# Performance work log

Hardware: AMD Instinct MI355X
Metric: run time of the kernel (lower is better)

The kernel has to match this reference:

```python
import jax, jax.numpy as jnp
import numpy as np

DIM = 512
NUM_LATENTS = 128
TRUE_BATCH = 8
DOWNSCALING = 16


def setup_inputs() -> dict:
    key = jax.random.key(0)
    ks = jax.random.split(key, 7)
    B = TRUE_BATCH * NUM_LATENTS
    s = 0.02
    return {
        "x": jax.random.normal(ks[0], (B, DOWNSCALING, DIM), dtype=jnp.float32),
        "l": jax.random.normal(ks[1], (B, NUM_LATENTS, DIM), dtype=jnp.float32),
        "Wq": jax.random.normal(ks[2], (DIM, DIM), dtype=jnp.float32) * s,
        "Wk": jax.random.normal(ks[3], (DIM, DIM), dtype=jnp.float32) * s,
        "Wv": jax.random.normal(ks[4], (DIM, DIM), dtype=jnp.float32) * s,
        "Wo": jax.random.normal(ks[5], (DIM, DIM), dtype=jnp.float32) * s,
        "bo": jax.random.normal(ks[6], (DIM,), dtype=jnp.float32) * s,
        "num_heads": 8,
    }


def reference(x, l, Wq, Wk, Wv, Wo, bo, num_heads):
    B, n_tok, d = x.shape
    num_latents = l.shape[1]
    dh = d // num_heads

    def split_heads(t):
        # (b, n, h*d) -> (b, h, n, d)
        b, n, _ = t.shape
        return t.reshape(b, n, num_heads, dh).transpose(0, 2, 1, 3)

    q = split_heads(x @ Wq.T)   # (B, h, n_tok, dh)
    k = split_heads(l @ Wk.T)   # (B, h, num_latents, dh)
    v = split_heads(l @ Wv.T)

    scores = jnp.einsum('bhid,bhjd->bhij', q, k) * (dh ** -0.5)

    # mask row for batch element b is row (b mod num_latents) of a causal triu mask:
    # latent index m may attend only to latents j <= m.
    row = jnp.arange(B) % num_latents                       # (B,)
    allowed = jnp.arange(num_latents)[None, :] <= row[:, None]  # (B, num_latents)
    mask = jnp.where(allowed, 0.0, -jnp.inf).astype(scores.dtype)

    scores = scores + mask[:, None, None, :]
    attn = jax.nn.softmax(scores, axis=-1)

    out = jnp.einsum('bhij,bhjd->bhid', attn, v)            # (B, h, n_tok, dh)
    out = out.transpose(0, 2, 1, 3).reshape(B, n_tok, d)
    return out @ Wo.T + bo
```

## Files before the change

kernel.cpp:

```cpp
#include <hip/hip_runtime.h>


typedef __bf16 bf16;
typedef __attribute__((ext_vector_type(8))) __bf16 bf16x8;
typedef __attribute__((ext_vector_type(4))) __bf16 bf16x4;
typedef __attribute__((ext_vector_type(4))) float  float4v;

#define MFMA16(a, b, c) __builtin_amdgcn_mfma_f32_16x16x32_bf16((a), (b), (c), 0, 0, 0)

__device__ __forceinline__ void gl2lds16(const bf16* g, bf16* l) {
    __builtin_amdgcn_global_load_lds(
        (const __attribute__((address_space(1))) void*)g,
        (__attribute__((address_space(3))) void*)l, 16, 0, 0);
}

__global__ __launch_bounds__(256) void cast_f32_bf16(const float* __restrict__ src,
                                                     bf16* __restrict__ dst, int n4) {
    const int stride = gridDim.x * 256;
    for (int i = blockIdx.x * 256 + threadIdx.x; i < n4; i += stride) {
        float4v f = ((const float4v*)src)[i];
        ((bf16x4*)dst)[i] = bf16x4{(bf16)f.x, (bf16)f.y, (bf16)f.z, (bf16)f.w};
    }
}

__global__ __launch_bounds__(256) void cast_weights(const float* __restrict__ Wq,
                                                    const float* __restrict__ Wk,
                                                    const float* __restrict__ Wv,
                                                    const float* __restrict__ Wo,
                                                    bf16* __restrict__ Wq_b,
                                                    bf16* __restrict__ Wkv_b,
                                                    bf16* __restrict__ Wo_b) {
    const int i = blockIdx.x * 256 + threadIdx.x;
    const int w = i >> 16;
    const int j = i & 65535;
    const float* src = (w == 0) ? Wq : (w == 1) ? Wk : (w == 2) ? Wv : Wo;
    bf16x4* dst = (w == 0) ? (bf16x4*)Wq_b
                : (w == 1) ? (bf16x4*)Wkv_b
                : (w == 2) ? ((bf16x4*)Wkv_b) + 65536
                           : (bf16x4*)Wo_b;
    float4v f = ((const float4v*)src)[j];
    dst[j] = bf16x4{(bf16)f.x, (bf16)f.y, (bf16)f.z, (bf16)f.w};
}

template <int MODE>
__global__ __launch_bounds__(256) void gemm_bt(const bf16* __restrict__ A,
                                               const bf16* __restrict__ W,
                                               void* __restrict__ C0,
                                               void* __restrict__ C1,
                                               const float* __restrict__ bias,
                                               int nT, int mPerXcd) {
    __shared__ alignas(16) bf16 Asl[128 * 32];
    __shared__ alignas(16) bf16 Bsl[128 * 32];

    const int bid = blockIdx.x;
    const int xcd = bid & 7;
    const int s   = bid >> 3;
    const int mt  = xcd * mPerXcd + s / nT;
    const int nt  = s % nT;
    const int m0  = mt * 128;
    const int n0  = nt * 128;

    const int tid  = threadIdx.x;
    const int wave = tid >> 6;
    const int lane = tid & 63;
    const int mi   = lane & 15;
    const int quad = lane >> 4;
    const int qrow = (wave >> 1) * 64;
    const int qcol = (wave & 1) * 64;

    const int srow = wave * 16 + (lane >> 2);
    const int scol = (lane & 3) * 8;

    float4v acc[4][4] = {};

    for (int kt = 0; kt < 16; ++kt) {
        const int k0 = kt * 32;
#pragma unroll
        for (int r = 0; r < 2; ++r) {
            gl2lds16(A + (size_t)(m0 + srow + r * 64) * 512 + k0 + scol,
                     &Asl[wave * 512 + r * 2048]);
            gl2lds16(W + (size_t)(n0 + srow + r * 64) * 512 + k0 + scol,
                     &Bsl[wave * 512 + r * 2048]);
        }
        __syncthreads();

        bf16x8 af[4], bfr[4];
#pragma unroll
        for (int i = 0; i < 4; ++i)
            af[i] = *(const bf16x8*)&Asl[(qrow + i * 16 + mi) * 32 + quad * 8];
#pragma unroll
        for (int j = 0; j < 4; ++j)
            bfr[j] = *(const bf16x8*)&Bsl[(qcol + j * 16 + mi) * 32 + quad * 8];
#pragma unroll
        for (int i = 0; i < 4; ++i)
#pragma unroll
            for (int j = 0; j < 4; ++j)
                acc[i][j] = MFMA16(af[i], bfr[j], acc[i][j]);
        __syncthreads();
    }

    if (MODE == 1 && nt >= 4) {
        const size_t b = (size_t)mt;
#pragma unroll
        for (int i = 0; i < 4; ++i) {
            const int lat0 = qrow + i * 16 + quad * 4;
#pragma unroll
            for (int j = 0; j < 4; ++j) {
                const int dd = (n0 - 512) + qcol + j * 16 + mi;
                bf16x4 o = {(bf16)acc[i][j][0], (bf16)acc[i][j][1],
                            (bf16)acc[i][j][2], (bf16)acc[i][j][3]};
                *(bf16x4*)((bf16*)C1 + (b * 512 + dd) * 128 + lat0) = o;
            }
        }
        return;
    }
#pragma unroll
    for (int i = 0; i < 4; ++i) {
#pragma unroll
        for (int j = 0; j < 4; ++j) {
            const int row = m0 + qrow + i * 16 + quad * 4;
            const int col = n0 + qcol + j * 16 + mi;
#pragma unroll
            for (int r = 0; r < 4; ++r) {
                float v = acc[i][j][r];
                if (MODE == 2)
                    ((float*)C0)[(size_t)(row + r) * 512 + col] = v + bias[col];
                else
                    ((bf16*)C0)[(size_t)(row + r) * 512 + col] = (bf16)v;
            }
        }
    }
}

__global__ __launch_bounds__(256) void attn_kernel(const bf16* __restrict__ Q,
                                                   const bf16* __restrict__ K,
                                                   const bf16* __restrict__ Vt,
                                                   bf16* __restrict__ O) {
    __shared__ alignas(16) bf16 Plds[4][16 * 136];

    const int w      = threadIdx.x >> 6;
    const int bh     = blockIdx.x * 4 + w;
    const int b      = bh >> 3;
    const int h      = bh & 7;
    const int rowb   = b & 127;
    const int ntiles = (rowb >> 4) + 1;
    const int nkt    = (ntiles + 1) >> 1;
    const int lane   = threadIdx.x & 63;
    const int mi     = lane & 15;
    const int quad   = lane >> 4;

    const bf16* qbase = Q + (size_t)(b * 16 + mi) * 512 + h * 64 + quad * 8;
    const bf16x8 aq0 = *(const bf16x8*)(qbase);
    const bf16x8 aq1 = *(const bf16x8*)(qbase + 32);

    float4v sc[8];
    const bf16* kbase = K + (size_t)(b * 128 + mi) * 512 + h * 64 + quad * 8;
#pragma unroll
    for (int jt = 0; jt < 8; ++jt) {
        if (jt < ntiles) {
            const bf16* kb = kbase + (size_t)jt * 16 * 512;
            bf16x8 bk0 = *(const bf16x8*)(kb);
            bf16x8 bk1 = *(const bf16x8*)(kb + 32);
            float4v a = {};
            a = MFMA16(aq0, bk0, a);
            a = MFMA16(aq1, bk1, a);
            sc[jt] = a;
        }
    }

#pragma unroll
    for (int jt = 0; jt < 8; ++jt) {
        if (jt < ntiles) {
            const bool masked = (jt * 16 + mi) > rowb;
#pragma unroll
            for (int r = 0; r < 4; ++r)
                sc[jt][r] = masked ? -1e30f : sc[jt][r] * 0.125f;
        }
    }

#pragma unroll
    for (int r = 0; r < 4; ++r) {
        float mx = sc[0][r];
#pragma unroll
        for (int jt = 1; jt < 8; ++jt)
            if (jt < ntiles) mx = fmaxf(mx, sc[jt][r]);
#pragma unroll
        for (int off = 1; off < 16; off <<= 1) mx = fmaxf(mx, __shfl_xor(mx, off, 64));
        float s = 0.f;
#pragma unroll
        for (int jt = 0; jt < 8; ++jt) {
            if (jt < ntiles) {
                float p = __expf(sc[jt][r] - mx);
                sc[jt][r] = p;
                s += p;
            }
        }
#pragma unroll
        for (int off = 1; off < 16; off <<= 1) s += __shfl_xor(s, off, 64);
        const float inv = 1.f / s;
#pragma unroll
        for (int jt = 0; jt < 8; ++jt) {
            if (jt < 2 * nkt) {
                float p = (jt < ntiles) ? sc[jt][r] * inv : 0.f;
                Plds[w][(quad * 4 + r) * 136 + jt * 16 + mi] = (bf16)p;
            }
        }
    }
    __syncthreads();

    float4v ao[4] = {};
    const bf16* vb0 = Vt + ((size_t)b * 512 + h * 64) * 128;
#pragma unroll
    for (int ks = 0; ks < 4; ++ks) {
        if (ks < nkt) {
            bf16x8 ap = *(const bf16x8*)&Plds[w][mi * 136 + ks * 32 + quad * 8];
#pragma unroll
            for (int jt = 0; jt < 4; ++jt) {
                bf16x8 bv = *(const bf16x8*)(vb0 + (size_t)(jt * 16 + mi) * 128
                                             + ks * 32 + quad * 8);
                ao[jt] = MFMA16(ap, bv, ao[jt]);
            }
        }
    }

#pragma unroll
    for (int jt = 0; jt < 4; ++jt)
#pragma unroll
        for (int r = 0; r < 4; ++r)
            O[(size_t)(b * 16 + quad * 4 + r) * 512 + h * 64 + jt * 16 + mi] =
                (bf16)ao[jt][r];
}

extern "C" void kernel_launch(void* const* d_in, const int* in_sizes, int n_in,
                              void* d_out, int out_size, void* d_ws, size_t ws_size,
                              hipStream_t stream) {
    const float* x  = (const float*)d_in[0];
    const float* l  = (const float*)d_in[1];
    const float* Wq = (const float*)d_in[2];
    const float* Wk = (const float*)d_in[3];
    const float* Wv = (const float*)d_in[4];
    const float* Wo = (const float*)d_in[5];
    const float* bo = (const float*)d_in[6];

    char* ws = (char*)d_ws;
    size_t off = 0;
    bf16* Wq_b  = (bf16*)(ws + off); off += (size_t)512 * 512 * 2;
    bf16* Wo_b  = (bf16*)(ws + off); off += (size_t)512 * 512 * 2;
    bf16* Wkv_b = (bf16*)(ws + off); off += (size_t)1024 * 512 * 2;
    bf16* xb    = (bf16*)(ws + off); off += (size_t)16384 * 512 * 2;
    bf16* lb    = (bf16*)(ws + off); off += (size_t)131072 * 512 * 2;
    bf16* Qb    = (bf16*)(ws + off); off += (size_t)16384 * 512 * 2;
    bf16* Kb    = (bf16*)(ws + off); off += (size_t)131072 * 512 * 2;
    bf16* Vtb   = (bf16*)(ws + off); off += (size_t)1024 * 512 * 128 * 2;
    bf16* AOb   = (bf16*)(ws + off);

    cast_weights<<<1024, 256, 0, stream>>>(Wq, Wk, Wv, Wo, Wq_b, Wkv_b, Wo_b);
    cast_f32_bf16<<<2048, 256, 0, stream>>>(x, xb, 16384 * 512 / 4);
    cast_f32_bf16<<<8192, 256, 0, stream>>>(l, lb, 131072 * 512 / 4);

    gemm_bt<0><<<512,  256, 0, stream>>>(xb, Wq_b,  Qb, nullptr, nullptr, 4, 16);
    gemm_bt<1><<<8192, 256, 0, stream>>>(lb, Wkv_b, Kb, Vtb,     nullptr, 8, 128);

    attn_kernel<<<2048, 256, 0, stream>>>(Qb, Kb, Vtb, AOb);

    gemm_bt<2><<<512, 256, 0, stream>>>(AOb, Wo_b, d_out, nullptr, bo, 4, 16);
}
```

Measured before the change: 713.3 us.

## Add dedicated 256x256 K/V projection GEMM with 4-stage LDS pipeline

Replaces the generic 128x128 K/V GEMM with a specialized kernel that computes 256x256 output tiles using 8 waves per block. It adds a 4-slot LDS ring filled by direct global-to-LDS loads, XOR swizzling to avoid bank conflicts, explicit waitcnt and barrier scheduling, and raised priority around the MFMA sections. The goal is more operand reuse per LDS byte and loads that overlap with compute in the largest GEMM. The cost is heavy LDS use of about 128 KB per block, which limits occupancy, plus fragile hand-written synchronization.

```diff
diff --git a/kernel.cpp b/kernel.cpp
--- a/kernel.cpp
+++ b/kernel.cpp
@@ -46,7 +46,6 @@
 __global__ __launch_bounds__(256) void gemm_bt(const bf16* __restrict__ A,
                                                const bf16* __restrict__ W,
                                                void* __restrict__ C0,
-                                               void* __restrict__ C1,
                                                const float* __restrict__ bias,
                                                int nT, int mPerXcd) {
     __shared__ alignas(16) bf16 Asl[128 * 32];
@@ -99,21 +98,6 @@
         __syncthreads();
     }
 
-    if (MODE == 1 && nt >= 4) {
-        const size_t b = (size_t)mt;
-#pragma unroll
-        for (int i = 0; i < 4; ++i) {
-            const int lat0 = qrow + i * 16 + quad * 4;
-#pragma unroll
-            for (int j = 0; j < 4; ++j) {
-                const int dd = (n0 - 512) + qcol + j * 16 + mi;
-                bf16x4 o = {(bf16)acc[i][j][0], (bf16)acc[i][j][1],
-                            (bf16)acc[i][j][2], (bf16)acc[i][j][3]};
-                *(bf16x4*)((bf16*)C1 + (b * 512 + dd) * 128 + lat0) = o;
-            }
-        }
-        return;
-    }
 #pragma unroll
     for (int i = 0; i < 4; ++i) {
 #pragma unroll
@@ -127,6 +111,122 @@
                     ((float*)C0)[(size_t)(row + r) * 512 + col] = v + bias[col];
                 else
                     ((bf16*)C0)[(size_t)(row + r) * 512 + col] = (bf16)v;
+            }
+        }
+    }
+}
+
+__global__ __launch_bounds__(512, 2) void gemm_kv(const bf16* __restrict__ A,
+                                                  const bf16* __restrict__ W,
+                                                  bf16* __restrict__ Kout,
+                                                  bf16* __restrict__ Vt) {
+    __shared__ alignas(16) bf16 As[4][256 * 32];
+    __shared__ alignas(16) bf16 Bs[4][256 * 32];
+
+    const int bid = blockIdx.x;
+    const int xcd = bid & 7;
+    const int s   = bid >> 3;
+    const int mt  = xcd * 64 + (s >> 2);
+    const int nt  = s & 3;
+    const int m0  = mt * 256;
+    const int n0  = nt * 256;
+
+    const int tid  = threadIdx.x;
+    const int wv   = tid >> 6;
+    const int lane = tid & 63;
+    const int wm   = wv >> 2;
+    const int wn   = wv & 3;
+    const int mi   = lane & 15;
+    const int quad = lane >> 4;
+
+    const int srow  = lane >> 2;
+    const int sunit = (lane & 3) ^ (srow & 3);
+    const bf16* gA = A + (size_t)(m0 + wv * 32 + srow) * 512 + sunit * 8;
+    const bf16* gB = W + (size_t)(n0 + wv * 32 + srow) * 512 + sunit * 8;
+    const int ldsOff0 = (wv * 32) * 32;
+    const int ldsOff1 = ldsOff0 + 16 * 32;
+
+    const int funit = (quad ^ (mi & 3)) * 8;
+    const int arow0 = wm * 128 + mi;
+    const int brow0 = wn * 64 + mi;
+
+    float4v acc[8][4] = {};
+
+#define KV_STAGE(t, ph)                                                        \
+    do {                                                                       \
+        const int _sl = (t) & 3;                                               \
+        gl2lds16(gA + (ph) * (16 * 512) + (t) * 32,                            \
+                 &As[_sl][(ph) ? ldsOff1 : ldsOff0]);                          \
+        gl2lds16(gB + (ph) * (16 * 512) + (t) * 32,                            \
+                 &Bs[_sl][(ph) ? ldsOff1 : ldsOff0]);                          \
+    } while (0)
+
+#pragma unroll
+    for (int t = 0; t < 3; ++t) { KV_STAGE(t, 0); KV_STAGE(t, 1); }
+    asm volatile("s_waitcnt vmcnt(8)" ::: "memory");
+    asm volatile("s_barrier" ::: "memory");
+
+    bf16x8 bfr[4];
+#pragma unroll
+    for (int t = 0; t < 16; ++t) {
+        const int sl = t & 3;
+#pragma unroll
+        for (int mh = 0; mh < 2; ++mh) {
+            bf16x8 af[4];
+#pragma unroll
+            for (int ii = 0; ii < 4; ++ii)
+                af[ii] = *(const bf16x8*)
+                    &As[sl][(arow0 + mh * 64 + ii * 16) * 32 + funit];
+            if (mh == 0) {
+#pragma unroll
+                for (int j = 0; j < 4; ++j)
+                    bfr[j] = *(const bf16x8*)&Bs[sl][(brow0 + j * 16) * 32 + funit];
+            }
+            if (t < 13) KV_STAGE(t + 3, mh);
+
+            asm volatile("s_barrier" ::: "memory");
+            asm volatile("s_waitcnt lgkmcnt(0)" ::: "memory");
+            __builtin_amdgcn_s_setprio(1);
+#pragma unroll
+            for (int ii = 0; ii < 4; ++ii)
+#pragma unroll
+                for (int j = 0; j < 4; ++j)
+                    acc[mh * 4 + ii][j] = MFMA16(af[ii], bfr[j], acc[mh * 4 + ii][j]);
+            __builtin_amdgcn_s_setprio(0);
+
+            if (mh == 1) {
+                if (t <= 12)      asm volatile("s_waitcnt vmcnt(8)" ::: "memory");
+                else if (t == 13) asm volatile("s_waitcnt vmcnt(4)" ::: "memory");
+                else if (t == 14) asm volatile("s_waitcnt vmcnt(0)" ::: "memory");
+            }
+            asm volatile("s_barrier" ::: "memory");
+        }
+    }
+#undef KV_STAGE
+
+    if (nt < 2) {
+#pragma unroll
+        for (int i = 0; i < 8; ++i) {
+            const int row = m0 + wm * 128 + i * 16 + quad * 4;
+#pragma unroll
+            for (int j = 0; j < 4; ++j) {
+                const int col = n0 + wn * 64 + j * 16 + mi;
+#pragma unroll
+                for (int r = 0; r < 4; ++r)
+                    Kout[(size_t)(row + r) * 512 + col] = (bf16)acc[i][j][r];
+            }
+        }
+    } else {
+        const size_t b = (size_t)mt * 2 + wm;
+#pragma unroll
+        for (int i = 0; i < 8; ++i) {
+            const int lat0 = i * 16 + quad * 4;
+#pragma unroll
+            for (int j = 0; j < 4; ++j) {
+                const int dd = (n0 - 512) + wn * 64 + j * 16 + mi;
+                bf16x4 o = {(bf16)acc[i][j][0], (bf16)acc[i][j][1],
+                            (bf16)acc[i][j][2], (bf16)acc[i][j][3]};
+                *(bf16x4*)(Vt + (b * 512 + dd) * 128 + lat0) = o;
             }
         }
     }
@@ -258,10 +358,10 @@
     cast_f32_bf16<<<2048, 256, 0, stream>>>(x, xb, 16384 * 512 / 4);
     cast_f32_bf16<<<8192, 256, 0, stream>>>(l, lb, 131072 * 512 / 4);
 
-    gemm_bt<0><<<512,  256, 0, stream>>>(xb, Wq_b,  Qb, nullptr, nullptr, 4, 16);
-    gemm_bt<1><<<8192, 256, 0, stream>>>(lb, Wkv_b, Kb, Vtb,     nullptr, 8, 128);
+    gemm_bt<0><<<512, 256, 0, stream>>>(xb, Wq_b, Qb, nullptr, 4, 16);
+    gemm_kv<<<2048, 512, 0, stream>>>(lb, Wkv_b, Kb, Vtb);
 
     attn_kernel<<<2048, 256, 0, stream>>>(Qb, Kb, Vtb, AOb);
 
-    gemm_bt<2><<<512, 256, 0, stream>>>(AOb, Wo_b, d_out, nullptr, bo, 4, 16);
-}
+    gemm_bt<2><<<512, 256, 0, stream>>>(AOb, Wo_b, d_out, bo, 4, 16);
+}
```

Result: no change. 718.9 us (+0.8%).
